# Performance work log

Measured on AMD Instinct MI355X. Metric: run time of the kernel, lower is better.

The kernel has to match this reference:

```python
import jax, jax.numpy as jnp
import numpy as np

T, B, D = 8192, 8, 512
PRIOR_COUNT = 2
EPS = 1e-5


def setup_inputs() -> dict:
    key = jax.random.key(0)
    ks = jax.random.split(key, 5)
    x = jax.random.normal(ks[0], (T, B, D), dtype=jnp.float32)
    padding_mask = jnp.zeros((B, T), dtype=bool)  # True = padded position
    prior_mean = jax.random.normal(ks[1], (D,), dtype=jnp.float32) * 0.1
    prior_logv = jax.random.normal(ks[2], (D,), dtype=jnp.float32) * 0.1
    weight = jax.random.normal(ks[3], (D,), dtype=jnp.float32) * 0.1
    bias = jax.random.normal(ks[4], (D,), dtype=jnp.float32) * 0.1
    return {"x": x, "prior_mean": prior_mean, "prior_logv": prior_logv,
            "weight": weight, "bias": bias, "padding_mask": padding_mask}


def reference(x, prior_mean, prior_logv, weight, bias, padding_mask):
    # x: (T, B, D); padding_mask: (B, T) with True = pad.
    # Per-timestep Welford running mean/variance (carried across time, skipping
    # padded steps) followed by affine normalization: the TimestepNorm forward.
    gamma = weight + 1.0
    beta = bias
    b = x.shape[1]
    count0 = jnp.full((b,), PRIOR_COUNT, dtype=x.dtype)
    mean0 = jnp.broadcast_to(prior_mean, (b, D)).astype(x.dtype)
    var0 = jnp.broadcast_to(jnp.exp(prior_logv), (b, D)).astype(x.dtype)
    mask_tb = padding_mask.T  # (T, B)

    def step(carry, inp):
        count, mean, var = carry
        xt, mt = inp                                  # xt: (B, D), mt: (B,)
        valid = (~mt).astype(xt.dtype)                # 1 if real token, 0 if pad
        c_new = count + valid
        coef = valid / c_new                          # 0 on padded steps
        delta = xt - mean
        mean_new = mean + coef[:, None] * delta
        # Welford variance update: var += (delta*(x - mean_new) - var)/count
        var_new = var + coef[:, None] * (delta * (xt - mean_new) - var)
        y = (xt - mean_new) * jax.lax.rsqrt(var_new + EPS) * gamma + beta
        return (c_new, mean_new, var_new), y

    (_, _, _), ys = jax.lax.scan(step, (count0, mean0, var0), (x, mask_tb))
    return ys  # (T, B, D), same layout as module output
```

## Files before the change

kernel.cpp:

```cpp
#include <hip/hip_runtime.h>
#include <math.h>


#define T_DIM 8192
#define B_DIM 8
#define D_DIM 512
#define BD    (B_DIM * D_DIM)
#define BD4   (BD / 4)
#define D4    (D_DIM / 4)
#define C0    2.0f
#define EPS   1e-5f

__device__ __forceinline__ float4 f4add(float4 a, float4 b) {
  return make_float4(a.x + b.x, a.y + b.y, a.z + b.z, a.w + b.w);
}
__device__ __forceinline__ float4 f4sub(float4 a, float4 b) {
  return make_float4(a.x - b.x, a.y - b.y, a.z - b.z, a.w - b.w);
}

template <int NC>
__global__ __launch_bounds__(128) void ts_pass1(
    const float* __restrict__ x, const unsigned char* __restrict__ mask,
    float* __restrict__ s1p, float* __restrict__ s2p, float* __restrict__ cnt) {
  constexpr int CT = T_DIM / NC;
  constexpr int NW = CT / 8;
  const int chunk = blockIdx.x;
  const int b     = blockIdx.y;
  const int tid   = threadIdx.x;
  const int t0    = chunk * CT;
  const float4* xp = (const float4*)x;

  unsigned long long mw[NW];
  const unsigned long long* m8 =
      (const unsigned long long*)(mask + b * T_DIM + t0);
#pragma unroll
  for (int j = 0; j < NW; ++j) mw[j] = m8[j];

  float4 s1 = make_float4(0.f, 0.f, 0.f, 0.f);
  float4 s2 = make_float4(0.f, 0.f, 0.f, 0.f);
  float c = 0.f;
#pragma unroll 8
  for (int i = 0; i < CT; ++i) {
    float valid = ((mw[i >> 3] >> ((i & 7) * 8)) & 0xffULL) ? 0.f : 1.f;
    float4 v = xp[(t0 + i) * BD4 + b * D4 + tid];
    c += valid;
    s1.x += valid * v.x; s2.x += valid * v.x * v.x;
    s1.y += valid * v.y; s2.y += valid * v.y * v.y;
    s1.z += valid * v.z; s2.z += valid * v.z * v.z;
    s1.w += valid * v.w; s2.w += valid * v.w * v.w;
  }
  const int pidx = chunk * BD4 + b * D4 + tid;
  ((float4*)s1p)[pidx] = s1;
  ((float4*)s2p)[pidx] = s2;
  if (tid == 0) cnt[chunk * B_DIM + b] = c;
}

template <int NC>
__global__ __launch_bounds__(256) void ts_pass2(
    float* __restrict__ s1p, float* __restrict__ s2p, float* __restrict__ cnt) {
  constexpr int KPL = NC / 64;
  const int wid  = (blockIdx.x * 256 + threadIdx.x) >> 6;
  const int lane = threadIdx.x & 63;

  if (wid < 2 * BD4) {
    float4* base = (float4*)(wid < BD4 ? s1p : s2p);
    const int col = wid & (BD4 - 1);
    float4 vals[KPL];
#pragma unroll
    for (int j = 0; j < KPL; ++j)
      vals[j] = base[(lane * KPL + j) * BD4 + col];
#pragma unroll
    for (int j = 1; j < KPL; ++j) vals[j] = f4add(vals[j], vals[j - 1]);
    float4 tot = vals[KPL - 1];
    float4 inc = tot;
#pragma unroll
    for (int off = 1; off < 64; off <<= 1) {
      float4 o;
      o.x = __shfl_up(inc.x, off);
      o.y = __shfl_up(inc.y, off);
      o.z = __shfl_up(inc.z, off);
      o.w = __shfl_up(inc.w, off);
      if (lane >= off) inc = f4add(inc, o);
    }
    float4 excl = f4sub(inc, tot);
#pragma unroll
    for (int j = KPL - 1; j >= 1; --j)
      base[(lane * KPL + j) * BD4 + col] = f4add(excl, vals[j - 1]);
    base[(lane * KPL) * BD4 + col] = excl;
  } else if (wid < 2 * BD4 + B_DIM) {
    const int b = wid - 2 * BD4;
    float vals[KPL];
#pragma unroll
    for (int j = 0; j < KPL; ++j) vals[j] = cnt[(lane * KPL + j) * B_DIM + b];
#pragma unroll
    for (int j = 1; j < KPL; ++j) vals[j] += vals[j - 1];
    float tot = vals[KPL - 1];
    float inc = tot;
#pragma unroll
    for (int off = 1; off < 64; off <<= 1) {
      float o = __shfl_up(inc, off);
      if (lane >= off) inc += o;
    }
    float excl = inc - tot;
#pragma unroll
    for (int j = KPL - 1; j >= 1; --j)
      cnt[(lane * KPL + j) * B_DIM + b] = excl + vals[j - 1];
    cnt[lane * KPL * B_DIM + b] = excl;
  }
}

template <int NC>
__global__ __launch_bounds__(128) void ts_pass3(
    const float* __restrict__ x, const unsigned char* __restrict__ mask,
    const float* __restrict__ pm, const float* __restrict__ plv,
    const float* __restrict__ w, const float* __restrict__ bias,
    const float* __restrict__ e1, const float* __restrict__ e2,
    const float* __restrict__ ecnt, float* __restrict__ out) {
  constexpr int CT = T_DIM / NC;
  constexpr int NW = CT / 8;
  const int chunk = blockIdx.x;
  const int b     = blockIdx.y;
  const int tid   = threadIdx.x;
  const int t0    = chunk * CT;
  const int col   = b * D4 + tid;

  float4 S1 = ((const float4*)e1)[chunk * BD4 + col];
  float4 S2 = ((const float4*)e2)[chunk * BD4 + col];
  float c = C0 + ecnt[chunk * B_DIM + b];

  float4 pm4 = ((const float4*)pm)[tid];
  float4 lv4 = ((const float4*)plv)[tid];
  float4 g4  = ((const float4*)w)[tid];
  float4 be4 = ((const float4*)bias)[tid];
  g4.x += 1.f; g4.y += 1.f; g4.z += 1.f; g4.w += 1.f;
  float M0x = C0 * pm4.x, M0y = C0 * pm4.y, M0z = C0 * pm4.z, M0w = C0 * pm4.w;
  float V2x = C0 * (__expf(lv4.x) + pm4.x * pm4.x);
  float V2y = C0 * (__expf(lv4.y) + pm4.y * pm4.y);
  float V2z = C0 * (__expf(lv4.z) + pm4.z * pm4.z);
  float V2w = C0 * (__expf(lv4.w) + pm4.w * pm4.w);

  unsigned long long mw[NW];
  const unsigned long long* m8 =
      (const unsigned long long*)(mask + b * T_DIM + t0);
#pragma unroll
  for (int j = 0; j < NW; ++j) mw[j] = m8[j];

  const float4* xp = (const float4*)x;
  float4* op = (float4*)out;

#pragma unroll 4
  for (int i = 0; i < CT; ++i) {
    float valid = ((mw[i >> 3] >> ((i & 7) * 8)) & 0xffULL) ? 0.f : 1.f;
    const int xi = (t0 + i) * BD4 + col;
    float4 v = xp[xi];
    c += valid;
    float rc = __builtin_amdgcn_rcpf(c);
    float4 y;
    {
      S1.x += valid * v.x; S2.x += valid * v.x * v.x;
      float M = M0x + S1.x;
      float mean = M * rc;
      float var = (V2x + S2.x - M * M * rc) * rc;
      y.x = (v.x - mean) * __builtin_amdgcn_rsqf(var + EPS) * g4.x + be4.x;
    }
    {
      S1.y += valid * v.y; S2.y += valid * v.y * v.y;
      float M = M0y + S1.y;
      float mean = M * rc;
      float var = (V2y + S2.y - M * M * rc) * rc;
      y.y = (v.y - mean) * __builtin_amdgcn_rsqf(var + EPS) * g4.y + be4.y;
    }
    {
      S1.z += valid * v.z; S2.z += valid * v.z * v.z;
      float M = M0z + S1.z;
      float mean = M * rc;
      float var = (V2z + S2.z - M * M * rc) * rc;
      y.z = (v.z - mean) * __builtin_amdgcn_rsqf(var + EPS) * g4.z + be4.z;
    }
    {
      S1.w += valid * v.w; S2.w += valid * v.w * v.w;
      float M = M0w + S1.w;
      float mean = M * rc;
      float var = (V2w + S2.w - M * M * rc) * rc;
      y.w = (v.w - mean) * __builtin_amdgcn_rsqf(var + EPS) * g4.w + be4.w;
    }
    op[xi] = y;
  }
}

template <int NC>
static void run_all(const float* x, const unsigned char* mask, const float* pm,
                    const float* plv, const float* w, const float* bias,
                    float* out, float* ws, hipStream_t stream) {
  float* s1p = ws;
  float* s2p = s1p + (size_t)NC * BD;
  float* cnt = s2p + (size_t)NC * BD;
  dim3 grid(NC, B_DIM);
  ts_pass1<NC><<<grid, 128, 0, stream>>>(x, mask, s1p, s2p, cnt);
  const int scan_waves = 2 * BD4 + B_DIM;
  const int scan_blocks = (scan_waves + 3) / 4;
  ts_pass2<NC><<<scan_blocks, 256, 0, stream>>>(s1p, s2p, cnt);
  ts_pass3<NC><<<grid, 128, 0, stream>>>(x, mask, pm, plv, w, bias, s1p, s2p,
                                         cnt, out);
}

extern "C" void kernel_launch(void* const* d_in, const int* in_sizes, int n_in,
                              void* d_out, int out_size, void* d_ws,
                              size_t ws_size, hipStream_t stream) {
  const float* x    = (const float*)d_in[0];
  const float* pm   = (const float*)d_in[1];
  const float* plv  = (const float*)d_in[2];
  const float* w    = (const float*)d_in[3];
  const float* bias = (const float*)d_in[4];
  const unsigned char* mask = (const unsigned char*)d_in[5];
  float* out = (float*)d_out;
  float* ws  = (float*)d_ws;

  const size_t need512 = ((size_t)2 * 512 * BD + 512 * B_DIM) * sizeof(float);
  const size_t need256 = ((size_t)2 * 256 * BD + 256 * B_DIM) * sizeof(float);
  if (ws_size >= need512) {
    run_all<512>(x, mask, pm, plv, w, bias, out, ws, stream);
  } else if (ws_size >= need256) {
    run_all<256>(x, mask, pm, plv, w, bias, out, ws, stream);
  } else {
    run_all<128>(x, mask, pm, plv, w, bias, out, ws, stream);
  }
}
```

Before: 284.6 us.

## Fuse three-pass scan into single-pass decoupled look-back kernel

Replaces the reduce / scan / normalize pipeline with one kernel. Each block keeps its chunk of x in registers, publishes its local sums with a flag, then walks back through predecessor flags (aggregate vs inclusive prefix) to obtain its exclusive prefix before normalizing. This aims to halve global reads of x and remove two launches plus the separate scan pass, at the cost of spin-waiting between blocks. Correctness depends on forward progress, i.e. earlier chunks being scheduled before the later ones that wait on them. The 16 float4 values held per thread also raise register pressure.

```diff
diff --git a/kernel.cpp b/kernel.cpp
--- a/kernel.cpp
+++ b/kernel.cpp
@@ -10,6 +10,178 @@
 #define D4    (D_DIM / 4)
 #define C0    2.0f
 #define EPS   1e-5f
+
+#define NCF   512
+#define CTF   (T_DIM / NCF)
+#define NWF   (CTF / 8)
+
+__global__ __launch_bounds__(256) void ts_init(int* __restrict__ flags) {
+  flags[blockIdx.x * 256 + threadIdx.x] = 0;
+}
+
+__global__ __launch_bounds__(128) void ts_fused(
+    const float* __restrict__ x, const unsigned char* __restrict__ mask,
+    const float* __restrict__ pm, const float* __restrict__ plv,
+    const float* __restrict__ w, const float* __restrict__ bias,
+    float* __restrict__ agg1, float* __restrict__ agg2,
+    float* __restrict__ aggc,
+    float* __restrict__ pre1, float* __restrict__ pre2,
+    float* __restrict__ prec,
+    int* __restrict__ flags, float* __restrict__ out) {
+  const int chunk = blockIdx.x;
+  const int b     = blockIdx.y;
+  const int tid   = threadIdx.x;
+  const int t0    = chunk * CTF;
+  const int col   = b * D4 + tid;
+  const int fidx  = chunk * B_DIM + b;
+
+  unsigned long long mw[NWF];
+  const unsigned long long* m8 =
+      (const unsigned long long*)(mask + b * T_DIM + t0);
+#pragma unroll
+  for (int j = 0; j < NWF; ++j) mw[j] = m8[j];
+
+  const float4* xp = (const float4*)x;
+  float4 xv[CTF];
+#pragma unroll
+  for (int i = 0; i < CTF; ++i) xv[i] = xp[(t0 + i) * BD4 + col];
+
+  float4 s1 = make_float4(0.f, 0.f, 0.f, 0.f);
+  float4 s2 = make_float4(0.f, 0.f, 0.f, 0.f);
+  float c = 0.f;
+#pragma unroll
+  for (int i = 0; i < CTF; ++i) {
+    float valid = ((mw[i >> 3] >> ((i & 7) * 8)) & 0xffULL) ? 0.f : 1.f;
+    float4 v = xv[i];
+    c += valid;
+    s1.x += valid * v.x; s2.x += valid * v.x * v.x;
+    s1.y += valid * v.y; s2.y += valid * v.y * v.y;
+    s1.z += valid * v.z; s2.z += valid * v.z * v.z;
+    s1.w += valid * v.w; s2.w += valid * v.w * v.w;
+  }
+
+  const int pidx = chunk * BD4 + col;
+  float4 R1 = make_float4(0.f, 0.f, 0.f, 0.f);
+  float4 R2 = make_float4(0.f, 0.f, 0.f, 0.f);
+  float Rc = 0.f;
+
+  if (chunk == 0) {
+    ((float4*)pre1)[pidx] = s1;
+    ((float4*)pre2)[pidx] = s2;
+    if (tid == 0) prec[fidx] = c;
+    __syncthreads();
+    if (tid == 0)
+      __hip_atomic_store(&flags[fidx], 2, __ATOMIC_RELEASE,
+                         __HIP_MEMORY_SCOPE_AGENT);
+  } else {
+    ((float4*)agg1)[pidx] = s1;
+    ((float4*)agg2)[pidx] = s2;
+    if (tid == 0) aggc[fidx] = c;
+    __syncthreads();
+    if (tid == 0)
+      __hip_atomic_store(&flags[fidx], 1, __ATOMIC_RELEASE,
+                         __HIP_MEMORY_SCOPE_AGENT);
+
+    __shared__ int sflag;
+    int k = chunk - 1;
+    for (;;) {
+      if (tid == 0) {
+        int st;
+        do {
+          st = __hip_atomic_load(&flags[k * B_DIM + b], __ATOMIC_RELAXED,
+                                 __HIP_MEMORY_SCOPE_AGENT);
+        } while (st == 0);
+        st = __hip_atomic_load(&flags[k * B_DIM + b], __ATOMIC_ACQUIRE,
+                               __HIP_MEMORY_SCOPE_AGENT);
+        sflag = st;
+      }
+      __syncthreads();
+      const int st = sflag;
+      __syncthreads();
+      const int kidx = k * BD4 + col;
+      if (st == 2) {
+        float4 a = ((const float4*)pre1)[kidx];
+        float4 d = ((const float4*)pre2)[kidx];
+        R1.x += a.x; R1.y += a.y; R1.z += a.z; R1.w += a.w;
+        R2.x += d.x; R2.y += d.y; R2.z += d.z; R2.w += d.w;
+        Rc += prec[k * B_DIM + b];
+        break;
+      }
+      float4 a = ((const float4*)agg1)[kidx];
+      float4 d = ((const float4*)agg2)[kidx];
+      R1.x += a.x; R1.y += a.y; R1.z += a.z; R1.w += a.w;
+      R2.x += d.x; R2.y += d.y; R2.z += d.z; R2.w += d.w;
+      Rc += aggc[k * B_DIM + b];
+      --k;
+    }
+
+    float4 P1, P2;
+    P1.x = R1.x + s1.x; P1.y = R1.y + s1.y;
+    P1.z = R1.z + s1.z; P1.w = R1.w + s1.w;
+    P2.x = R2.x + s2.x; P2.y = R2.y + s2.y;
+    P2.z = R2.z + s2.z; P2.w = R2.w + s2.w;
+    ((float4*)pre1)[pidx] = P1;
+    ((float4*)pre2)[pidx] = P2;
+    if (tid == 0) prec[fidx] = Rc + c;
+    __syncthreads();
+    if (tid == 0)
+      __hip_atomic_store(&flags[fidx], 2, __ATOMIC_RELEASE,
+                         __HIP_MEMORY_SCOPE_AGENT);
+  }
+
+  float4 pm4 = ((const float4*)pm)[tid];
+  float4 lv4 = ((const float4*)plv)[tid];
+  float4 g4  = ((const float4*)w)[tid];
+  float4 be4 = ((const float4*)bias)[tid];
+  g4.x += 1.f; g4.y += 1.f; g4.z += 1.f; g4.w += 1.f;
+  float M0x = C0 * pm4.x, M0y = C0 * pm4.y, M0z = C0 * pm4.z, M0w = C0 * pm4.w;
+  float V2x = C0 * (__expf(lv4.x) + pm4.x * pm4.x);
+  float V2y = C0 * (__expf(lv4.y) + pm4.y * pm4.y);
+  float V2z = C0 * (__expf(lv4.z) + pm4.z * pm4.z);
+  float V2w = C0 * (__expf(lv4.w) + pm4.w * pm4.w);
+
+  float4 S1 = R1, S2 = R2;
+  float c2 = C0 + Rc;
+  float4* op = (float4*)out;
+
+#pragma unroll
+  for (int i = 0; i < CTF; ++i) {
+    float valid = ((mw[i >> 3] >> ((i & 7) * 8)) & 0xffULL) ? 0.f : 1.f;
+    float4 v = xv[i];
+    c2 += valid;
+    float rc = __builtin_amdgcn_rcpf(c2);
+    float4 y;
+    {
+      S1.x += valid * v.x; S2.x += valid * v.x * v.x;
+      float M = M0x + S1.x;
+      float mean = M * rc;
+      float var = (V2x + S2.x - M * M * rc) * rc;
+      y.x = (v.x - mean) * __builtin_amdgcn_rsqf(var + EPS) * g4.x + be4.x;
+    }
+    {
+      S1.y += valid * v.y; S2.y += valid * v.y * v.y;
+      float M = M0y + S1.y;
+      float mean = M * rc;
+      float var = (V2y + S2.y - M * M * rc) * rc;
+      y.y = (v.y - mean) * __builtin_amdgcn_rsqf(var + EPS) * g4.y + be4.y;
+    }
+    {
+      S1.z += valid * v.z; S2.z += valid * v.z * v.z;
+      float M = M0z + S1.z;
+      float mean = M * rc;
+      float var = (V2z + S2.z - M * M * rc) * rc;
+      y.z = (v.z - mean) * __builtin_amdgcn_rsqf(var + EPS) * g4.z + be4.z;
+    }
+    {
+      S1.w += valid * v.w; S2.w += valid * v.w * v.w;
+      float M = M0w + S1.w;
+      float mean = M * rc;
+      float var = (V2w + S2.w - M * M * rc) * rc;
+      y.w = (v.w - mean) * __builtin_amdgcn_rsqf(var + EPS) * g4.w + be4.w;
+    }
+    op[(t0 + i) * BD4 + col] = y;
+  }
+}
 
 __device__ __forceinline__ float4 f4add(float4 a, float4 b) {
   return make_float4(a.x + b.x, a.y + b.y, a.z + b.z, a.w + b.w);
@@ -189,9 +361,10 @@
 }
 
 template <int NC>
-static void run_all(const float* x, const unsigned char* mask, const float* pm,
-                    const float* plv, const float* w, const float* bias,
-                    float* out, float* ws, hipStream_t stream) {
+static void run_3pass(const float* x, const unsigned char* mask,
+                      const float* pm, const float* plv, const float* w,
+                      const float* bias, float* out, float* ws,
+                      hipStream_t stream) {
   float* s1p = ws;
   float* s2p = s1p + (size_t)NC * BD;
   float* cnt = s2p + (size_t)NC * BD;
@@ -216,13 +389,32 @@
   float* out = (float*)d_out;
   float* ws  = (float*)d_ws;
 
+  const size_t fused_floats = (size_t)4 * NCF * BD + 2 * NCF * B_DIM;
+  const size_t need_fused = fused_floats * sizeof(float) +
+                            (size_t)NCF * B_DIM * sizeof(int);
+  if (ws_size >= need_fused) {
+    float* agg1 = ws;
+    float* agg2 = agg1 + (size_t)NCF * BD;
+    float* pre1 = agg2 + (size_t)NCF * BD;
+    float* pre2 = pre1 + (size_t)NCF * BD;
+    float* aggc = pre2 + (size_t)NCF * BD;
+    float* prec = aggc + (size_t)NCF * B_DIM;
+    int*   flags = (int*)(prec + (size_t)NCF * B_DIM);
+
+    ts_init<<<(NCF * B_DIM) / 256, 256, 0, stream>>>(flags);
+    dim3 grid(NCF, B_DIM);
+    ts_fused<<<grid, 128, 0, stream>>>(x, mask, pm, plv, w, bias, agg1, agg2,
+                                       aggc, pre1, pre2, prec, flags, out);
+    return;
+  }
+
   const size_t need512 = ((size_t)2 * 512 * BD + 512 * B_DIM) * sizeof(float);
   const size_t need256 = ((size_t)2 * 256 * BD + 256 * B_DIM) * sizeof(float);
   if (ws_size >= need512) {
-    run_all<512>(x, mask, pm, plv, w, bias, out, ws, stream);
+    run_3pass<512>(x, mask, pm, plv, w, bias, out, ws, stream);
   } else if (ws_size >= need256) {
-    run_all<256>(x, mask, pm, plv, w, bias, out, ws, stream);
+    run_3pass<256>(x, mask, pm, plv, w, bias, out, ws, stream);
   } else {
-    run_all<128>(x, mask, pm, plv, w, bias, out, ws, stream);
-  }
-}
+    run_3pass<128>(x, mask, pm, plv, w, bias, out, ws, stream);
+  }
+}
```

Measured after the change: 1.088 ms. 3.82x slower.
